# Optimization experiments

Measured on AMD Instinct MI355X. Metric: run time of the kernel, lower is better.

## Reference

```python
import jax, jax.numpy as jnp
import numpy as np

N = 512     # nodes
E = 16384   # edges (N * avg_degree 32, unique pairs)
F = 64      # nedgeinput
FO = 64     # nedgeoutput


def setup_inputs() -> dict:
    key = jax.random.key(0)
    ks = jax.random.split(key, 7)
    # unique edge pairs so scatter-assign is well-defined
    perm = jax.random.permutation(ks[0], N * N)[:E]
    edge_index = jnp.stack([perm // N, perm % N]).astype(jnp.int32)  # [2, E]
    C = jax.random.normal(ks[1], (E, F), dtype=jnp.float32)
    batch_node = jax.random.normal(ks[2], (N,), dtype=jnp.float32)
    s = 1.0 / np.sqrt(F)
    W_L1 = jax.random.normal(ks[3], (F, F), dtype=jnp.float32) * s          # Linear(F, F), weight [out,in]
    W_L2 = jax.random.normal(ks[4], (F, F), dtype=jnp.float32) * s
    W_mlp1 = jax.random.normal(ks[5], (8 * F, 2 * F), dtype=jnp.float32) * (1.0 / np.sqrt(2 * F))
    W_mlp2 = jax.random.normal(ks[6], (FO, 8 * F), dtype=jnp.float32) * (1.0 / np.sqrt(8 * F))
    return {"edge_index": edge_index, "C": C, "batch_node": batch_node,
            "W_L1": W_L1, "W_L2": W_L2, "W_mlp1": W_mlp1, "W_mlp2": W_mlp2}


def reference(edge_index, C, batch_node, W_L1, W_L2, W_mlp1, W_mlp2):
    n = batch_node.shape[0]
    f = C.shape[1]
    ei0, ei1 = edge_index[0], edge_index[1]
    X = C @ W_L1.T  # [E, F]  (L1(C))
    Y = C @ W_L2.T  # [E, F]  (L2(C))
    # scatter edges into dense [F, N, N] adjacency-like tensors
    resx = jnp.zeros((f, n, n), dtype=C.dtype).at[:, ei0, ei1].set(X.T)
    resy = jnp.zeros((f, n, n), dtype=C.dtype).at[:, ei0, ei1].set(Y.T)
    # batched dense matmul per feature channel, then gather back at edges
    res = jnp.einsum('fij,fjk->fik', resx, resy)  # [F, N, N]
    tmp_matmul = res[:, ei0, ei1].T  # [E, F]
    tmp = jnp.concatenate([C, tmp_matmul], axis=1)  # [E, 2F]
    return jax.nn.relu(tmp @ W_mlp1.T) @ W_mlp2.T  # [E, FO]
```

## Files before the change

### kernel.cpp

```cpp
#include <hip/hip_runtime.h>

#define NN 512
#define NE 16384
#define NF 64

typedef __attribute__((ext_vector_type(8))) short short8_t;
typedef __attribute__((ext_vector_type(4))) float float4_t;

__device__ inline unsigned short f2bf(float f) {
  unsigned u = __builtin_bit_cast(unsigned, f);
  u += 0x7fff + ((u >> 16) & 1);
  return (unsigned short)(u >> 16);
}

__global__ __launch_bounds__(256) void k_init(const float* __restrict__ Wm1,
                                              const float* __restrict__ Wm2,
                                              uint4* __restrict__ tabs,
                                              unsigned short* __restrict__ W1B,
                                              unsigned short* __restrict__ W2B) {
  int t = blockIdx.x * 256 + threadIdx.x;
  uint4 m1 = make_uint4(~0u, ~0u, ~0u, ~0u);
  tabs[t] = m1;
  tabs[t + 65536] = m1;
  if (t < 16384) {
    float4 v = ((const float4*)Wm1)[t];
    short4 s;
    s.x = f2bf(v.x); s.y = f2bf(v.y); s.z = f2bf(v.z); s.w = f2bf(v.w);
    ((short4*)W1B)[t] = s;
  } else if (t < 24576) {
    int i = t - 16384;
    float4 v = ((const float4*)Wm2)[i];
    short4 s;
    s.x = f2bf(v.x); s.y = f2bf(v.y); s.z = f2bf(v.z); s.w = f2bf(v.w);
    ((short4*)W2B)[i] = s;
  }
}

__global__ __launch_bounds__(256) void k_xy_mfma(const float* __restrict__ C,
                                                 const float* __restrict__ W1,
                                                 const float* __restrict__ W2,
                                                 const int* __restrict__ ei,
                                                 int* __restrict__ eid,
                                                 int* __restrict__ eidT,
                                                 float* __restrict__ X,
                                                 float* __restrict__ Y,
                                                 unsigned short* __restrict__ tmpB) {
  __shared__ __attribute__((aligned(16))) short W1s[64 * 72];
  __shared__ __attribute__((aligned(16))) short W2s[64 * 72];
  int t = threadIdx.x;
  int w = t >> 6;
  int lane = t & 63;
  int col = lane & 15;
  int q = lane >> 4;
  int base_e = blockIdx.x * 64 + w * 16;

  if (t < 64) {
    int e = blockIdx.x * 64 + t;
    int i = ei[e];
    int k = ei[NE + e];
    eid[i * NN + k] = e;
    eidT[k * NN + i] = e;
  }

#pragma unroll
  for (int z = 0; z < 4; z++) {
    int gi = z * 256 + t;
    int r = gi >> 4, c = gi & 15;
    float4 v1 = ((const float4*)W1)[r * 16 + c];
    float4 v2 = ((const float4*)W2)[r * 16 + c];
    short4 s1, s2;
    s1.x = f2bf(v1.x); s1.y = f2bf(v1.y); s1.z = f2bf(v1.z); s1.w = f2bf(v1.w);
    s2.x = f2bf(v2.x); s2.y = f2bf(v2.y); s2.z = f2bf(v2.z); s2.w = f2bf(v2.w);
    *(short4*)(W1s + r * 72 + c * 4) = s1;
    *(short4*)(W2s + r * 72 + c * 4) = s2;
  }
  __syncthreads();

  short8_t bfrag[2];
#pragma unroll
  for (int ks = 0; ks < 2; ks++) {
    float4 c0 = ((const float4*)C)[(size_t)(base_e + col) * 16 + ks * 8 + q * 2];
    float4 c1 = ((const float4*)C)[(size_t)(base_e + col) * 16 + ks * 8 + q * 2 + 1];
    short8_t s;
    s[0] = (short)f2bf(c0.x); s[1] = (short)f2bf(c0.y);
    s[2] = (short)f2bf(c0.z); s[3] = (short)f2bf(c0.w);
    s[4] = (short)f2bf(c1.x); s[5] = (short)f2bf(c1.y);
    s[6] = (short)f2bf(c1.z); s[7] = (short)f2bf(c1.w);
    bfrag[ks] = s;
    *(short8_t*)(tmpB + (size_t)(base_e + col) * 128 + ks * 32 + q * 8) = s;
  }

  float4_t xa[4], ya[4];
#pragma unroll
  for (int ft = 0; ft < 4; ft++) {
    xa[ft] = (float4_t){0.f, 0.f, 0.f, 0.f};
    ya[ft] = (float4_t){0.f, 0.f, 0.f, 0.f};
  }
#pragma unroll
  for (int ks = 0; ks < 2; ks++) {
#pragma unroll
    for (int ft = 0; ft < 4; ft++) {
      short8_t a1 = *(const short8_t*)(W1s + (ft * 16 + col) * 72 + ks * 32 + q * 8);
      short8_t a2 = *(const short8_t*)(W2s + (ft * 16 + col) * 72 + ks * 32 + q * 8);
      xa[ft] = __builtin_amdgcn_mfma_f32_16x16x32_bf16(a1, bfrag[ks], xa[ft], 0, 0, 0);
      ya[ft] = __builtin_amdgcn_mfma_f32_16x16x32_bf16(a2, bfrag[ks], ya[ft], 0, 0, 0);
    }
  }
#pragma unroll
  for (int ft = 0; ft < 4; ft++) {
    float4 vx = make_float4(xa[ft][0], xa[ft][1], xa[ft][2], xa[ft][3]);
    float4 vy = make_float4(ya[ft][0], ya[ft][1], ya[ft][2], ya[ft][3]);
    *(float4*)(X + (size_t)(base_e + col) * 64 + ft * 16 + q * 4) = vx;
    *(float4*)(Y + (size_t)(base_e + col) * 64 + ft * 16 + q * 4) = vy;
  }
}

__global__ __launch_bounds__(256) void k_spmm(const int* __restrict__ ei,
                                              const int* __restrict__ eid,
                                              const int* __restrict__ eidT,
                                              const float* __restrict__ X,
                                              const float* __restrict__ Y,
                                              unsigned short* __restrict__ tmpB) {
  int lane = threadIdx.x & 63;
  int e = (blockIdx.x * 256 + threadIdx.x) >> 6;
  int i = ei[e];
  int k = ei[NE + e];
  const int* rowI = eid + (size_t)i * NN;
  const int* rowK = eidT + (size_t)k * NN;
  float acc = 0.f;
#pragma unroll
  for (int jb = 0; jb < NN; jb += 64) {
    int e1 = rowI[jb + lane];
    int e2 = rowK[jb + lane];
    unsigned long long m = __ballot((e1 >= 0) && (e2 >= 0));
    while (m) {
      int src = (int)__builtin_ctzll(m);
      m &= m - 1;
      int s1 = __shfl(e1, src);
      int s2 = __shfl(e2, src);
      acc = fmaf(X[(size_t)s1 * 64 + lane], Y[(size_t)s2 * 64 + lane], acc);
    }
  }
  tmpB[(size_t)e * 128 + 64 + lane] = f2bf(acc);
}

__global__ __launch_bounds__(256) void k_mlp2(
    const unsigned short* __restrict__ tmpB,
    const unsigned short* __restrict__ W1B,
    const unsigned short* __restrict__ W2B,
    float* __restrict__ out) {
  __shared__ __attribute__((aligned(16))) short W1s[128 * 136];
  __shared__ __attribute__((aligned(16))) short W2s[64 * 136];
  __shared__ __attribute__((aligned(16))) short hS[4][16 * 72];

  int t = threadIdx.x;
  int w = t >> 6;
  int lane = t & 63;
  int col = lane & 15;
  int q = lane >> 4;
  int g = w & 1;
  int h = w >> 1;
  int base_e = blockIdx.x * 32 + g * 16;

  short8_t btmp[4];
#pragma unroll
  for (int ks = 0; ks < 4; ks++)
    btmp[ks] = *(const short8_t*)(tmpB + (size_t)(base_e + col) * 128 + ks * 32 + q * 8);

  float4_t oacc[4];
#pragma unroll
  for (int ft = 0; ft < 4; ft++) oacc[ft] = (float4_t){0.f, 0.f, 0.f, 0.f};

  for (int it = 0; it < 4; it++) {
    __syncthreads();
    {
      uint4* d1 = (uint4*)W1s;
      const uint4* s1 = (const uint4*)W1B;
#pragma unroll
      for (int z = 0; z < 8; z++) {
        int gi = z * 256 + t;
        int r = gi >> 4, c = gi & 15;
        int grow = ((r >> 6) * 4 + it) * 64 + (r & 63);
        d1[r * 17 + c] = s1[(size_t)grow * 16 + c];
      }
      uint4* d2 = (uint4*)W2s;
      const uint4* s2 = (const uint4*)W2B;
#pragma unroll
      for (int z = 0; z < 4; z++) {
        int gi = z * 256 + t;
        int r = gi >> 4, c = gi & 15;
        int gc = ((c >> 3) * 4 + it) * 8 + (c & 7);
        d2[r * 17 + c] = s2[(size_t)r * 64 + gc];
      }
    }
    __syncthreads();

#pragma unroll
    for (int ht = 0; ht < 4; ht++) {
      float4_t hacc = (float4_t){0.f, 0.f, 0.f, 0.f};
#pragma unroll
      for (int ks = 0; ks < 4; ks++) {
        short8_t af = *(const short8_t*)(W1s + (h * 64 + ht * 16 + col) * 136 + ks * 32 + q * 8);
        hacc = __builtin_amdgcn_mfma_f32_16x16x32_bf16(af, btmp[ks], hacc, 0, 0, 0);
      }
      short4 hp;
      hp.x = (short)f2bf(fmaxf(hacc[0], 0.f));
      hp.y = (short)f2bf(fmaxf(hacc[1], 0.f));
      hp.z = (short)f2bf(fmaxf(hacc[2], 0.f));
      hp.w = (short)f2bf(fmaxf(hacc[3], 0.f));
      *(short4*)(&hS[w][col * 72 + ht * 16 + q * 4]) = hp;
    }

#pragma unroll
    for (int ks2 = 0; ks2 < 2; ks2++) {
      short8_t a2 = *(const short8_t*)(&hS[w][col * 72 + ks2 * 32 + q * 8]);
#pragma unroll
      for (int ft = 0; ft < 4; ft++) {
        short8_t b2 = *(const short8_t*)(W2s + (ft * 16 + col) * 136 + h * 64 + ks2 * 32 + q * 8);
        oacc[ft] = __builtin_amdgcn_mfma_f32_16x16x32_bf16(a2, b2, oacc[ft], 0, 0, 0);
      }
    }
  }

  __syncthreads();
  float* red = (float*)W1s;
  if (h == 1) {
#pragma unroll
    for (int ft = 0; ft < 4; ft++)
#pragma unroll
      for (int r = 0; r < 4; r++)
        red[(g * 16 + q * 4 + r) * 66 + ft * 16 + col] = oacc[ft][r];
  }
  __syncthreads();
  if (h == 0) {
#pragma unroll
    for (int ft = 0; ft < 4; ft++)
#pragma unroll
      for (int r = 0; r < 4; r++) {
        float v = oacc[ft][r] + red[(g * 16 + q * 4 + r) * 66 + ft * 16 + col];
        out[(size_t)(base_e + q * 4 + r) * 64 + ft * 16 + col] = v;
      }
  }
}

extern "C" void kernel_launch(void* const* d_in, const int* in_sizes, int n_in,
                              void* d_out, int out_size, void* d_ws, size_t ws_size,
                              hipStream_t stream) {
  const int* ei = (const int*)d_in[0];
  const float* C = (const float*)d_in[1];
  const float* W1 = (const float*)d_in[3];
  const float* W2 = (const float*)d_in[4];
  const float* Wm1 = (const float*)d_in[5];
  const float* Wm2 = (const float*)d_in[6];
  float* out = (float*)d_out;

  char* p = (char*)d_ws;
  int* eid = (int*)p;                 p += (size_t)NN * NN * 4;
  int* eidT = (int*)p;                p += (size_t)NN * NN * 4;
  float* X = (float*)p;               p += (size_t)NE * NF * 4;
  float* Y = (float*)p;               p += (size_t)NE * NF * 4;
  unsigned short* tmpB = (unsigned short*)p;  p += (size_t)NE * 128 * 2;
  unsigned short* W1B = (unsigned short*)p;   p += (size_t)512 * 128 * 2;
  unsigned short* W2B = (unsigned short*)p;   p += (size_t)64 * 512 * 2;

  k_init<<<256, 256, 0, stream>>>(Wm1, Wm2, (uint4*)eid, W1B, W2B);
  k_xy_mfma<<<NE / 64, 256, 0, stream>>>(C, W1, W2, ei, eid, eidT, X, Y, tmpB);
  k_spmm<<<(NE * 64) / 256, 256, 0, stream>>>(ei, eid, eidT, X, Y, tmpB);
  k_mlp2<<<NE / 32, 256, 0, stream>>>(tmpB, W1B, W2B, out);
}
```

Baseline: 99.28 us.

## Replace dense edge-id row scans with bitmask adjacency intersection and bf16 X/Y

The builder kernel now also sets per-node 512-bit out/in adjacency bitmasks with atomicOr. The sparse product kernel ANDs the two 16-word masks for each edge and loads edge ids only for the common neighbours, instead of scanning two full 512-entry id rows. Because only masked entries are read, the dense -1 initialisation of the id tables is dropped, and only the small mask buffer is zeroed. X and Y are also stored as bf16 to halve gather traffic, at the cost of extra rounding before the product.

```diff
diff --git a/kernel.cpp b/kernel.cpp
--- a/kernel.cpp
+++ b/kernel.cpp
@@ -12,17 +12,19 @@
   u += 0x7fff + ((u >> 16) & 1);
   return (unsigned short)(u >> 16);
 }
+__device__ inline float bf2f(unsigned short u) {
+  unsigned v = ((unsigned)u) << 16;
+  return __builtin_bit_cast(float, v);
+}
 
 __global__ __launch_bounds__(256) void k_init(const float* __restrict__ Wm1,
                                               const float* __restrict__ Wm2,
-                                              uint4* __restrict__ tabs,
+                                              unsigned* __restrict__ masks,
                                               unsigned short* __restrict__ W1B,
                                               unsigned short* __restrict__ W2B) {
   int t = blockIdx.x * 256 + threadIdx.x;
-  uint4 m1 = make_uint4(~0u, ~0u, ~0u, ~0u);
-  tabs[t] = m1;
-  tabs[t + 65536] = m1;
   if (t < 16384) {
+    masks[t] = 0u;
     float4 v = ((const float4*)Wm1)[t];
     short4 s;
     s.x = f2bf(v.x); s.y = f2bf(v.y); s.z = f2bf(v.z); s.w = f2bf(v.w);
@@ -42,8 +44,10 @@
                                                  const int* __restrict__ ei,
                                                  int* __restrict__ eid,
                                                  int* __restrict__ eidT,
-                                                 float* __restrict__ X,
-                                                 float* __restrict__ Y,
+                                                 unsigned* __restrict__ maskO,
+                                                 unsigned* __restrict__ maskI,
+                                                 unsigned short* __restrict__ Xb,
+                                                 unsigned short* __restrict__ Yb,
                                                  unsigned short* __restrict__ tmpB) {
   __shared__ __attribute__((aligned(16))) short W1s[64 * 72];
   __shared__ __attribute__((aligned(16))) short W2s[64 * 72];
@@ -60,6 +64,8 @@
     int k = ei[NE + e];
     eid[i * NN + k] = e;
     eidT[k * NN + i] = e;
+    atomicOr(&maskO[i * 16 + (k >> 5)], 1u << (k & 31));
+    atomicOr(&maskI[k * 16 + (i >> 5)], 1u << (i & 31));
   }
 
 #pragma unroll
@@ -108,37 +114,45 @@
   }
 #pragma unroll
   for (int ft = 0; ft < 4; ft++) {
-    float4 vx = make_float4(xa[ft][0], xa[ft][1], xa[ft][2], xa[ft][3]);
-    float4 vy = make_float4(ya[ft][0], ya[ft][1], ya[ft][2], ya[ft][3]);
-    *(float4*)(X + (size_t)(base_e + col) * 64 + ft * 16 + q * 4) = vx;
-    *(float4*)(Y + (size_t)(base_e + col) * 64 + ft * 16 + q * 4) = vy;
+    short4 sx, sy;
+    sx.x = (short)f2bf(xa[ft][0]); sx.y = (short)f2bf(xa[ft][1]);
+    sx.z = (short)f2bf(xa[ft][2]); sx.w = (short)f2bf(xa[ft][3]);
+    sy.x = (short)f2bf(ya[ft][0]); sy.y = (short)f2bf(ya[ft][1]);
+    sy.z = (short)f2bf(ya[ft][2]); sy.w = (short)f2bf(ya[ft][3]);
+    *(short4*)(Xb + (size_t)(base_e + col) * 64 + ft * 16 + q * 4) = sx;
+    *(short4*)(Yb + (size_t)(base_e + col) * 64 + ft * 16 + q * 4) = sy;
   }
 }
 
 __global__ __launch_bounds__(256) void k_spmm(const int* __restrict__ ei,
                                               const int* __restrict__ eid,
                                               const int* __restrict__ eidT,
-                                              const float* __restrict__ X,
-                                              const float* __restrict__ Y,
+                                              const unsigned* __restrict__ maskO,
+                                              const unsigned* __restrict__ maskI,
+                                              const unsigned short* __restrict__ Xb,
+                                              const unsigned short* __restrict__ Yb,
                                               unsigned short* __restrict__ tmpB) {
   int lane = threadIdx.x & 63;
   int e = (blockIdx.x * 256 + threadIdx.x) >> 6;
   int i = ei[e];
   int k = ei[NE + e];
-  const int* rowI = eid + (size_t)i * NN;
-  const int* rowK = eidT + (size_t)k * NN;
+  unsigned mm = 0;
+  if (lane < 16) mm = maskO[i * 16 + lane] & maskI[k * 16 + lane];
+  unsigned long long has = __ballot(mm != 0);
   float acc = 0.f;
-#pragma unroll
-  for (int jb = 0; jb < NN; jb += 64) {
-    int e1 = rowI[jb + lane];
-    int e2 = rowK[jb + lane];
-    unsigned long long m = __ballot((e1 >= 0) && (e2 >= 0));
-    while (m) {
-      int src = (int)__builtin_ctzll(m);
-      m &= m - 1;
-      int s1 = __shfl(e1, src);
-      int s2 = __shfl(e2, src);
-      acc = fmaf(X[(size_t)s1 * 64 + lane], Y[(size_t)s2 * 64 + lane], acc);
+  while (has) {
+    int l = (int)__builtin_ctzll(has);
+    has &= has - 1;
+    unsigned bits = __shfl(mm, l);
+    while (bits) {
+      int b = __builtin_ctz(bits);
+      bits &= bits - 1;
+      int j = l * 32 + b;
+      int s1 = eid[i * NN + j];
+      int s2 = eidT[k * NN + j];
+      float xv = bf2f(Xb[(size_t)s1 * 64 + lane]);
+      float yv = bf2f(Yb[(size_t)s2 * 64 + lane]);
+      acc = fmaf(xv, yv, acc);
     }
   }
   tmpB[(size_t)e * 128 + 64 + lane] = f2bf(acc);
@@ -257,14 +271,17 @@
   char* p = (char*)d_ws;
   int* eid = (int*)p;                 p += (size_t)NN * NN * 4;
   int* eidT = (int*)p;                p += (size_t)NN * NN * 4;
-  float* X = (float*)p;               p += (size_t)NE * NF * 4;
-  float* Y = (float*)p;               p += (size_t)NE * NF * 4;
+  unsigned* masks = (unsigned*)p;     p += (size_t)16384 * 4;
+  unsigned short* Xb = (unsigned short*)p;    p += (size_t)NE * NF * 2;
+  unsigned short* Yb = (unsigned short*)p;    p += (size_t)NE * NF * 2;
   unsigned short* tmpB = (unsigned short*)p;  p += (size_t)NE * 128 * 2;
   unsigned short* W1B = (unsigned short*)p;   p += (size_t)512 * 128 * 2;
   unsigned short* W2B = (unsigned short*)p;   p += (size_t)64 * 512 * 2;
-
-  k_init<<<256, 256, 0, stream>>>(Wm1, Wm2, (uint4*)eid, W1B, W2B);
-  k_xy_mfma<<<NE / 64, 256, 0, stream>>>(C, W1, W2, ei, eid, eidT, X, Y, tmpB);
-  k_spmm<<<(NE * 64) / 256, 256, 0, stream>>>(ei, eid, eidT, X, Y, tmpB);
+  unsigned* maskO = masks;
+  unsigned* maskI = masks + 8192;
+
+  k_init<<<128, 256, 0, stream>>>(Wm1, Wm2, masks, W1B, W2B);
+  k_xy_mfma<<<NE / 64, 256, 0, stream>>>(C, W1, W2, ei, eid, eidT, maskO, maskI, Xb, Yb, tmpB);
+  k_spmm<<<(NE * 64) / 256, 256, 0, stream>>>(ei, eid, eidT, maskO, maskI, Xb, Yb, tmpB);
   k_mlp2<<<NE / 32, 256, 0, stream>>>(tmpB, W1B, W2B, out);
 }
```

New measurement: 98.26 us. No clear change (-1.0%).
